# Performance work log

Measured on AMD Instinct MI355X. Metric: run time of the kernel, lower is better.

Reference implementation:

```python
import jax, jax.numpy as jnp
import numpy as np

N, K, D = 32768, 8192, 64  # active voxels, codebook size, embedding dim


def setup_inputs() -> dict:
    key = jax.random.key(0)
    k1, k2 = jax.random.split(key)
    z_feats = jax.random.normal(k1, (N, D), dtype=jnp.float32)
    codebook = jax.random.normal(k2, (K, D), dtype=jnp.float32)  # nn.Embedding weight, N(0,1)
    return {"z_feats": z_feats, "codebook": codebook}


def reference(z_feats, codebook):
    # torch.cdist(z, E) followed by argmin(dim=1). sqrt is monotonic, so argmin over
    # squared Euclidean distances gives identical indices (same math, cheaper).
    # d2[n,k] = ||z_n||^2 - 2 z_n . e_k + ||e_k||^2  -> [N, K] (dominant intermediate)
    d2 = (jnp.sum(z_feats * z_feats, axis=1, keepdims=True)
          - 2.0 * (z_feats @ codebook.T)
          + jnp.sum(codebook * codebook, axis=1))
    encoding_indices = jnp.argmin(d2, axis=1)  # [N]

    quantized_feats = codebook[encoding_indices]  # embedding gather [N, D]

    # F.mse_loss == mean over all elements
    commitment_loss = jnp.mean((z_feats - jax.lax.stop_gradient(quantized_feats)) ** 2)
    vq_loss = jnp.mean((quantized_feats - jax.lax.stop_gradient(z_feats)) ** 2)

    # straight-through estimator
    quantized = z_feats + jax.lax.stop_gradient(quantized_feats - z_feats)
    return quantized, vq_loss, commitment_loss, encoding_indices
```

## Files before the change

### kernel.cpp

```cpp
#include <hip/hip_runtime.h>
#include <cfloat>


typedef __bf16 bf16x8 __attribute__((ext_vector_type(8)));
typedef float  f32x16 __attribute__((ext_vector_type(16)));

constexpr int N_ROWS = 32768;
constexpr int K_CB   = 8192;
constexpr int D_DIM  = 64;
constexpr size_t NQ  = (size_t)N_ROWS * D_DIM;
constexpr int WS_LOSS = K_CB;
constexpr size_t WS_SPLIT_F   = 8448;
constexpr size_t SPLIT_BYTES  = (size_t)K_CB * D_DIM * 4;
constexpr size_t WS_NEED      = WS_SPLIT_F * 4 + SPLIT_BYTES;
constexpr int NROUND = K_CB / 256;

#define GLL16(gp, lp)                                                          \
  __builtin_amdgcn_global_load_lds(                                            \
      (const __attribute__((address_space(1))) unsigned int*)(gp),             \
      (__attribute__((address_space(3))) unsigned int*)(lp), 16, 0, 0)

__global__ __launch_bounds__(256) void vq_prep(const float* __restrict__ cb,
                                               float* __restrict__ ws) {
  const int k = blockIdx.x * 256 + threadIdx.x;
  if (k == 0) ws[WS_LOSS] = 0.0f;
  const float4* p = reinterpret_cast<const float4*>(cb) + (size_t)k * 16;
  float s0 = 0.f, s1 = 0.f, s2 = 0.f, s3 = 0.f;
#pragma unroll
  for (int j = 0; j < 16; ++j) {
    float4 v = p[j];
    s0 = fmaf(v.x, v.x, s0); s1 = fmaf(v.y, v.y, s1);
    s2 = fmaf(v.z, v.z, s2); s3 = fmaf(v.w, v.w, s3);
  }
  ws[k] = (s0 + s1) + (s2 + s3);
}

__global__ __launch_bounds__(256) void vq_split(const float* __restrict__ cb,
                                                float* __restrict__ ws) {
  const int u  = blockIdx.x * 256 + threadIdx.x;
  const int k  = u >> 3, ch = u & 7;
  const int r  = k >> 8, t = (k >> 5) & 7, c = k & 31;
  const float* src = cb + (size_t)k * D_DIM + ch * 8;
  float4 f0 = *reinterpret_cast<const float4*>(src);
  float4 f1 = *reinterpret_cast<const float4*>(src + 4);
  float xs[8] = {f0.x, f0.y, f0.z, f0.w, f1.x, f1.y, f1.z, f1.w};
  bf16x8 hi, lo;
#pragma unroll
  for (int j = 0; j < 8; ++j) {
    __bf16 h = (__bf16)xs[j];
    hi[j] = h;
    lo[j] = (__bf16)(xs[j] - (float)h);
  }
  char* base = reinterpret_cast<char*>(ws + WS_SPLIT_F) +
               (size_t)r * 65536 + (size_t)t * 8192 + (size_t)ch * 512 + (size_t)c * 16;
  *reinterpret_cast<bf16x8*>(base)        = hi;
  *reinterpret_cast<bf16x8*>(base + 4096) = lo;
}

__global__ __launch_bounds__(512, 2) void vq_mfma(const float* __restrict__ z,
                                                  const float* __restrict__ cb,
                                                  float* __restrict__ ws,
                                                  float* __restrict__ out) {
  __shared__ __attribute__((aligned(16))) unsigned char lds[131072];

  const int tid = threadIdx.x;
  const int w = tid >> 6, l = tid & 63;
  const int c = l & 31, g = l >> 5;
  const int rowbase = blockIdx.x * 128;

  bf16x8 zh[4][4], zl[4][4];
#pragma unroll
  for (int q = 0; q < 4; ++q) {
    const float* zr = z + (size_t)(rowbase + q * 32 + c) * D_DIM + 8 * g;
#pragma unroll
    for (int s = 0; s < 4; ++s) {
      float4 f0 = *reinterpret_cast<const float4*>(zr + 16 * s);
      float4 f1 = *reinterpret_cast<const float4*>(zr + 16 * s + 4);
      float xs[8] = {f0.x, f0.y, f0.z, f0.w, f1.x, f1.y, f1.z, f1.w};
#pragma unroll
      for (int j = 0; j < 8; ++j) {
        __bf16 h = (__bf16)xs[j];
        zh[q][s][j] = h;
        zl[q][s][j] = (__bf16)(xs[j] - (float)h);
      }
    }
  }

  const char* sg = reinterpret_cast<const char*>(ws + WS_SPLIT_F) +
                   (size_t)w * 1024 + (size_t)l * 16;

#pragma unroll
  for (int j = 0; j < 8; ++j) GLL16(sg + j * 8192, lds + j * 8192 + w * 1024);
  __syncthreads();

  float best[4];
  int   bpack[4];
#pragma unroll
  for (int q = 0; q < 4; ++q) { best[q] = FLT_MAX; bpack[q] = 0; }

  for (int r = 0; r < NROUND; ++r) {
    const int buf = r & 1;
    if (r < NROUND - 1) {
      const char* s2 = sg + (size_t)(r + 1) * 65536;
      unsigned db = (unsigned)(buf ^ 1) * 65536u;
#pragma unroll
      for (int j = 0; j < 8; ++j)
        GLL16(s2 + j * 8192, lds + db + j * 8192 + w * 1024);
    }

    const unsigned rb = (unsigned)buf * 65536u + (unsigned)w * 8192u +
                        (unsigned)g * 512u + (unsigned)c * 16u;
    f32x16 a0, a1, a2, a3;
#pragma unroll
    for (int i = 0; i < 16; ++i) { a0[i] = 0.f; a1[i] = 0.f; a2[i] = 0.f; a3[i] = 0.f; }

#pragma unroll
    for (int s = 0; s < 4; ++s) {
      bf16x8 ca = *reinterpret_cast<const bf16x8*>(lds + rb + s * 1024);
      bf16x8 cb_ = *reinterpret_cast<const bf16x8*>(lds + rb + s * 1024 + 4096);
      a0 = __builtin_amdgcn_mfma_f32_32x32x16_bf16(ca, zh[0][s], a0, 0, 0, 0);
      a1 = __builtin_amdgcn_mfma_f32_32x32x16_bf16(ca, zh[1][s], a1, 0, 0, 0);
      a2 = __builtin_amdgcn_mfma_f32_32x32x16_bf16(ca, zh[2][s], a2, 0, 0, 0);
      a3 = __builtin_amdgcn_mfma_f32_32x32x16_bf16(ca, zh[3][s], a3, 0, 0, 0);
      a0 = __builtin_amdgcn_mfma_f32_32x32x16_bf16(ca, zl[0][s], a0, 0, 0, 0);
      a1 = __builtin_amdgcn_mfma_f32_32x32x16_bf16(ca, zl[1][s], a1, 0, 0, 0);
      a2 = __builtin_amdgcn_mfma_f32_32x32x16_bf16(ca, zl[2][s], a2, 0, 0, 0);
      a3 = __builtin_amdgcn_mfma_f32_32x32x16_bf16(ca, zl[3][s], a3, 0, 0, 0);
      a0 = __builtin_amdgcn_mfma_f32_32x32x16_bf16(cb_, zh[0][s], a0, 0, 0, 0);
      a1 = __builtin_amdgcn_mfma_f32_32x32x16_bf16(cb_, zh[1][s], a1, 0, 0, 0);
      a2 = __builtin_amdgcn_mfma_f32_32x32x16_bf16(cb_, zh[2][s], a2, 0, 0, 0);
      a3 = __builtin_amdgcn_mfma_f32_32x32x16_bf16(cb_, zh[3][s], a3, 0, 0, 0);
    }

    const float* rp = ws + r * 256 + w * 32 + 4 * g;
    float4 rv0 = *reinterpret_cast<const float4*>(rp);
    float4 rv1 = *reinterpret_cast<const float4*>(rp + 8);
    float4 rv2 = *reinterpret_cast<const float4*>(rp + 16);
    float4 rv3 = *reinterpret_cast<const float4*>(rp + 24);
    float r2v[16] = {rv0.x, rv0.y, rv0.z, rv0.w, rv1.x, rv1.y, rv1.z, rv1.w,
                     rv2.x, rv2.y, rv2.z, rv2.w, rv3.x, rv3.y, rv3.z, rv3.w};
    const int pb = r << 4;
#pragma unroll
    for (int i = 0; i < 16; ++i) {
      float s0 = fmaf(-2.f, a0[i], r2v[i]);
      float s1 = fmaf(-2.f, a1[i], r2v[i]);
      float s2 = fmaf(-2.f, a2[i], r2v[i]);
      float s3 = fmaf(-2.f, a3[i], r2v[i]);
      if (s0 < best[0]) { best[0] = s0; bpack[0] = pb + i; }
      if (s1 < best[1]) { best[1] = s1; bpack[1] = pb + i; }
      if (s2 < best[2]) { best[2] = s2; bpack[2] = pb + i; }
      if (s3 < best[3]) { best[3] = s3; bpack[3] = pb + i; }
    }
    __syncthreads();
  }

  int bk[4];
#pragma unroll
  for (int q = 0; q < 4; ++q) {
    int rr = bpack[q] >> 4, i = bpack[q] & 15;
    int cid = (i & 3) + 8 * (i >> 2) + 4 * g;
    bk[q] = rr * 256 + w * 32 + cid;
  }
#pragma unroll
  for (int q = 0; q < 4; ++q) {
    float ob = __shfl_xor(best[q], 32, 64);
    int   ok = __shfl_xor(bk[q], 32, 64);
    if (ob < best[q] || (ob == best[q] && ok < bk[q])) { best[q] = ob; bk[q] = ok; }
  }

  float* fbuf = reinterpret_cast<float*>(lds);
  int*   kbuf = reinterpret_cast<int*>(lds + 4096);
  int*   ibuf = reinterpret_cast<int*>(lds + 8192);
  if (l < 32) {
#pragma unroll
    for (int q = 0; q < 4; ++q) {
      fbuf[w * 128 + q * 32 + l] = best[q];
      kbuf[w * 128 + q * 32 + l] = bk[q];
    }
  }
  __syncthreads();

  if (tid < 128) {
    float bb = fbuf[tid];
    int   kk = kbuf[tid];
#pragma unroll
    for (int ww = 1; ww < 8; ++ww) {
      float b2 = fbuf[ww * 128 + tid];
      int   k2 = kbuf[ww * 128 + tid];
      if (b2 < bb || (b2 == bb && k2 < kk)) { bb = b2; kk = k2; }
    }
    ibuf[tid] = kk;
    out[NQ + 2 + rowbase + tid] = (float)kk;
  }
  __syncthreads();

  {
    const int row_l = tid >> 2, seg = tid & 3;
    const int idx  = ibuf[row_l];
    const int grow = rowbase + row_l;
    const float4* qp = reinterpret_cast<const float4*>(cb + (size_t)idx * D_DIM + seg * 16);
    const float4* zp = reinterpret_cast<const float4*>(z + (size_t)grow * D_DIM + seg * 16);
    float4*       op = reinterpret_cast<float4*>(out + (size_t)grow * D_DIM + seg * 16);
    float lp = 0.f;
#pragma unroll
    for (int cc = 0; cc < 4; ++cc) {
      float4 qv = qp[cc], zv = zp[cc];
      op[cc] = qv;
      float dx = zv.x - qv.x, dy = zv.y - qv.y;
      float dz = zv.z - qv.z, dw = zv.w - qv.w;
      lp += (dx * dx + dy * dy) + (dz * dz + dw * dw);
    }
#pragma unroll
    for (int off = 32; off > 0; off >>= 1) lp += __shfl_down(lp, off, 64);
    if (l == 0) atomicAdd(ws + WS_LOSS, lp);
  }
}

__global__ __launch_bounds__(512, 2) void vq_main_reg(const float* __restrict__ z,
                                                      const float* __restrict__ cb,
                                                      float* __restrict__ ws,
                                                      float* __restrict__ out) {
  __shared__ __attribute__((aligned(16))) unsigned char lds[65536];
  const int tid = threadIdx.x;
  const int w = tid >> 6, l = tid & 63;
  const int rg = w >> 1, sp = w & 1;
  const int c = l & 31, g = l >> 5;
  const int rowbase = blockIdx.x * 128;
  const int myrow = rowbase + rg * 32 + c;

  bf16x8 zh[4], zl[4];
#pragma unroll
  for (int s = 0; s < 4; ++s) {
    const float* zp = z + (size_t)myrow * D_DIM + 16 * s + 8 * g;
    float4 f0 = *reinterpret_cast<const float4*>(zp);
    float4 f1 = *reinterpret_cast<const float4*>(zp + 4);
    float xs[8] = {f0.x, f0.y, f0.z, f0.w, f1.x, f1.y, f1.z, f1.w};
#pragma unroll
    for (int j = 0; j < 8; ++j) {
      __bf16 h = (__bf16)xs[j];
      zh[s][j] = h;
      zl[s][j] = (__bf16)(xs[j] - (float)h);
    }
  }
  const int st_t01 = tid >> 8;
  const int st_c   = (tid >> 3) & 31;
  const int st_ch  = tid & 7;
  const unsigned st_off = (unsigned)(st_t01 * 16384 + st_ch * 512 + st_c * 16);
  const float* st_g = cb + (size_t)(st_t01 * 32 + st_c) * D_DIM + st_ch * 8;

  float best = FLT_MAX;
  int   bidx = 0;
  float4 p0 = *reinterpret_cast<const float4*>(st_g);
  float4 p1 = *reinterpret_cast<const float4*>(st_g + 4);
  {
    float xs[8] = {p0.x, p0.y, p0.z, p0.w, p1.x, p1.y, p1.z, p1.w};
    bf16x8 hi, lo;
#pragma unroll
    for (int j = 0; j < 8; ++j) {
      __bf16 h = (__bf16)xs[j];
      hi[j] = h; lo[j] = (__bf16)(xs[j] - (float)h);
    }
    *reinterpret_cast<bf16x8*>(lds + st_off)        = hi;
    *reinterpret_cast<bf16x8*>(lds + st_off + 8192) = lo;
  }
  __syncthreads();
  const unsigned rd_base = (unsigned)(sp * 16384 + c * 16);
  for (int r = 0; r < 128; ++r) {
    const int buf = r & 1;
    if (r < 127) {
      const float* gp = st_g + (size_t)(r + 1) * (64 * D_DIM);
      p0 = *reinterpret_cast<const float4*>(gp);
      p1 = *reinterpret_cast<const float4*>(gp + 4);
    }
    const unsigned b0 = (unsigned)buf * 32768u + rd_base;
    bf16x8 ch[4], cl[4];
#pragma unroll
    for (int s = 0; s < 4; ++s) {
      unsigned off = b0 + (unsigned)((2 * s + g) * 512);
      ch[s] = *reinterpret_cast<const bf16x8*>(lds + off);
      cl[s] = *reinterpret_cast<const bf16x8*>(lds + off + 8192);
    }
    f32x16 acc;
#pragma unroll
    for (int i = 0; i < 16; ++i) acc[i] = 0.f;
#pragma unroll
    for (int s = 0; s < 4; ++s) {
      acc = __builtin_amdgcn_mfma_f32_32x32x16_bf16(ch[s], zh[s], acc, 0, 0, 0);
      acc = __builtin_amdgcn_mfma_f32_32x32x16_bf16(ch[s], zl[s], acc, 0, 0, 0);
      acc = __builtin_amdgcn_mfma_f32_32x32x16_bf16(cl[s], zh[s], acc, 0, 0, 0);
    }
    const int tb = (2 * r + sp) * 32 + 4 * g;
#pragma unroll
    for (int q = 0; q < 4; ++q) {
      float4 rv = *reinterpret_cast<const float4*>(ws + tb + 8 * q);
      float ra[4] = {rv.x, rv.y, rv.z, rv.w};
#pragma unroll
      for (int j = 0; j < 4; ++j) {
        float sc = fmaf(-2.f, acc[4 * q + j], ra[j]);
        int kg = tb + 8 * q + j;
        if (sc < best) { best = sc; bidx = kg; }
      }
    }
    if (r < 127) {
      float xs[8] = {p0.x, p0.y, p0.z, p0.w, p1.x, p1.y, p1.z, p1.w};
      bf16x8 hi, lo;
#pragma unroll
      for (int j = 0; j < 8; ++j) {
        __bf16 h = (__bf16)xs[j];
        hi[j] = h; lo[j] = (__bf16)(xs[j] - (float)h);
      }
      unsigned wo = (unsigned)(buf ^ 1) * 32768u + st_off;
      *reinterpret_cast<bf16x8*>(lds + wo)        = hi;
      *reinterpret_cast<bf16x8*>(lds + wo + 8192) = lo;
    }
    __syncthreads();
  }
  {
    float ob = __shfl_xor(best, 32, 64);
    int   oi = __shfl_xor(bidx, 32, 64);
    if (ob < best || (ob == best && oi < bidx)) { best = ob; bidx = oi; }
  }
  float* mf  = reinterpret_cast<float*>(lds);
  int*   mi  = reinterpret_cast<int*>(lds + 1024);
  int*   mix = reinterpret_cast<int*>(lds + 2048);
  if (l < 32) { mf[w * 32 + c] = best; mi[w * 32 + c] = bidx; }
  __syncthreads();
  if (tid < 128) {
    int rgg = tid >> 5, rl = tid & 31;
    float b0 = mf[(2 * rgg) * 32 + rl];     int i0 = mi[(2 * rgg) * 32 + rl];
    float b1 = mf[(2 * rgg + 1) * 32 + rl]; int i1 = mi[(2 * rgg + 1) * 32 + rl];
    int idx = (b1 < b0 || (b1 == b0 && i1 < i0)) ? i1 : i0;
    mix[tid] = idx;
    out[NQ + 2 + rowbase + tid] = (float)idx;
  }
  __syncthreads();
  {
    const int row_l = tid >> 2, seg = tid & 3;
    const int idx  = mix[row_l];
    const int grow = rowbase + row_l;
    const float4* qp = reinterpret_cast<const float4*>(cb + (size_t)idx * D_DIM + seg * 16);
    const float4* zp = reinterpret_cast<const float4*>(z + (size_t)grow * D_DIM + seg * 16);
    float4*       op = reinterpret_cast<float4*>(out + (size_t)grow * D_DIM + seg * 16);
    float lp = 0.f;
#pragma unroll
    for (int cc = 0; cc < 4; ++cc) {
      float4 qv = qp[cc], zv = zp[cc];
      op[cc] = qv;
      float dx = zv.x - qv.x, dy = zv.y - qv.y;
      float dz = zv.z - qv.z, dw = zv.w - qv.w;
      lp += (dx * dx + dy * dy) + (dz * dz + dw * dw);
    }
#pragma unroll
    for (int off = 32; off > 0; off >>= 1) lp += __shfl_down(lp, off, 64);
    if (l == 0) atomicAdd(ws + WS_LOSS, lp);
  }
}

__global__ void vq_fin(const float* __restrict__ ws, float* __restrict__ out) {
  float mm = ws[WS_LOSS] * (1.0f / (float)(N_ROWS * D_DIM));
  out[NQ]     = mm;
  out[NQ + 1] = mm;
}

extern "C" void kernel_launch(void* const* d_in, const int* in_sizes, int n_in,
                              void* d_out, int out_size, void* d_ws, size_t ws_size,
                              hipStream_t stream) {
  (void)in_sizes; (void)n_in; (void)out_size;
  const float* z  = (const float*)d_in[0];
  const float* cb = (const float*)d_in[1];
  float* out = (float*)d_out;
  float* ws  = (float*)d_ws;

  vq_prep<<<K_CB / 256, 256, 0, stream>>>(cb, ws);
  if (ws_size >= WS_NEED) {
    vq_split<<<256, 256, 0, stream>>>(cb, ws);
    vq_mfma<<<N_ROWS / 128, 512, 0, stream>>>(z, cb, ws, out);
  } else {
    vq_main_reg<<<N_ROWS / 128, 512, 0, stream>>>(z, cb, ws, out);
  }
  vq_fin<<<1, 1, 0, stream>>>(ws, out);
}
```

Measured before the change: 144.7 us.

## Halve rows per block and drop LDS double buffering to raise occupancy

The MFMA kernel now handles 64 rows per block instead of 128, uses a single 64 KB LDS buffer instead of a 128 KB double buffer, and declares 4 blocks per CU in launch bounds instead of 2. Each round loads its codebook tile, synchronizes, then computes. Latency hiding now comes from more resident blocks rather than software prefetch. MFMA sections are wrapped in s_setprio to favour matrix issue. In exchange, each block reuses the loaded codebook tile across half as many rows, so total codebook traffic from L2 doubles, and every round now waits on a load with a barrier instead of overlapping it.

```diff
diff --git a/kernel.cpp b/kernel.cpp
--- a/kernel.cpp
+++ b/kernel.cpp
@@ -57,20 +57,20 @@
   *reinterpret_cast<bf16x8*>(base + 4096) = lo;
 }
 
-__global__ __launch_bounds__(512, 2) void vq_mfma(const float* __restrict__ z,
-                                                  const float* __restrict__ cb,
-                                                  float* __restrict__ ws,
-                                                  float* __restrict__ out) {
-  __shared__ __attribute__((aligned(16))) unsigned char lds[131072];
+__global__ __launch_bounds__(512, 4) void vq_mfma8(const float* __restrict__ z,
+                                                   const float* __restrict__ cb,
+                                                   float* __restrict__ ws,
+                                                   float* __restrict__ out) {
+  __shared__ __attribute__((aligned(16))) unsigned char lds[65536];
 
   const int tid = threadIdx.x;
   const int w = tid >> 6, l = tid & 63;
   const int c = l & 31, g = l >> 5;
-  const int rowbase = blockIdx.x * 128;
-
-  bf16x8 zh[4][4], zl[4][4];
-#pragma unroll
-  for (int q = 0; q < 4; ++q) {
+  const int rowbase = blockIdx.x * 64;
+
+  bf16x8 zh[2][4], zl[2][4];
+#pragma unroll
+  for (int q = 0; q < 2; ++q) {
     const float* zr = z + (size_t)(rowbase + q * 32 + c) * D_DIM + 8 * g;
 #pragma unroll
     for (int s = 0; s < 4; ++s) {
@@ -89,48 +89,34 @@
   const char* sg = reinterpret_cast<const char*>(ws + WS_SPLIT_F) +
                    (size_t)w * 1024 + (size_t)l * 16;
 
-#pragma unroll
-  for (int j = 0; j < 8; ++j) GLL16(sg + j * 8192, lds + j * 8192 + w * 1024);
-  __syncthreads();
-
-  float best[4];
-  int   bpack[4];
-#pragma unroll
-  for (int q = 0; q < 4; ++q) { best[q] = FLT_MAX; bpack[q] = 0; }
+  float best0 = FLT_MAX, best1 = FLT_MAX;
+  int   bp0 = 0, bp1 = 0;
 
   for (int r = 0; r < NROUND; ++r) {
-    const int buf = r & 1;
-    if (r < NROUND - 1) {
-      const char* s2 = sg + (size_t)(r + 1) * 65536;
-      unsigned db = (unsigned)(buf ^ 1) * 65536u;
-#pragma unroll
-      for (int j = 0; j < 8; ++j)
-        GLL16(s2 + j * 8192, lds + db + j * 8192 + w * 1024);
-    }
-
-    const unsigned rb = (unsigned)buf * 65536u + (unsigned)w * 8192u +
-                        (unsigned)g * 512u + (unsigned)c * 16u;
-    f32x16 a0, a1, a2, a3;
-#pragma unroll
-    for (int i = 0; i < 16; ++i) { a0[i] = 0.f; a1[i] = 0.f; a2[i] = 0.f; a3[i] = 0.f; }
-
+    const char* s2 = sg + (size_t)r * 65536;
+#pragma unroll
+    for (int j = 0; j < 8; ++j)
+      GLL16(s2 + j * 8192, lds + j * 8192 + w * 1024);
+    __syncthreads();
+
+    const unsigned rb = (unsigned)w * 8192u + (unsigned)g * 512u + (unsigned)c * 16u;
+    f32x16 a0, a1;
+#pragma unroll
+    for (int i = 0; i < 16; ++i) { a0[i] = 0.f; a1[i] = 0.f; }
+
+    __builtin_amdgcn_s_setprio(1);
 #pragma unroll
     for (int s = 0; s < 4; ++s) {
       bf16x8 ca = *reinterpret_cast<const bf16x8*>(lds + rb + s * 1024);
-      bf16x8 cb_ = *reinterpret_cast<const bf16x8*>(lds + rb + s * 1024 + 4096);
+      bf16x8 cl = *reinterpret_cast<const bf16x8*>(lds + rb + s * 1024 + 4096);
       a0 = __builtin_amdgcn_mfma_f32_32x32x16_bf16(ca, zh[0][s], a0, 0, 0, 0);
       a1 = __builtin_amdgcn_mfma_f32_32x32x16_bf16(ca, zh[1][s], a1, 0, 0, 0);
-      a2 = __builtin_amdgcn_mfma_f32_32x32x16_bf16(ca, zh[2][s], a2, 0, 0, 0);
-      a3 = __builtin_amdgcn_mfma_f32_32x32x16_bf16(ca, zh[3][s], a3, 0, 0, 0);
       a0 = __builtin_amdgcn_mfma_f32_32x32x16_bf16(ca, zl[0][s], a0, 0, 0, 0);
       a1 = __builtin_amdgcn_mfma_f32_32x32x16_bf16(ca, zl[1][s], a1, 0, 0, 0);
-      a2 = __builtin_amdgcn_mfma_f32_32x32x16_bf16(ca, zl[2][s], a2, 0, 0, 0);
-      a3 = __builtin_amdgcn_mfma_f32_32x32x16_bf16(ca, zl[3][s], a3, 0, 0, 0);
-      a0 = __builtin_amdgcn_mfma_f32_32x32x16_bf16(cb_, zh[0][s], a0, 0, 0, 0);
-      a1 = __builtin_amdgcn_mfma_f32_32x32x16_bf16(cb_, zh[1][s], a1, 0, 0, 0);
-      a2 = __builtin_amdgcn_mfma_f32_32x32x16_bf16(cb_, zh[2][s], a2, 0, 0, 0);
-      a3 = __builtin_amdgcn_mfma_f32_32x32x16_bf16(cb_, zh[3][s], a3, 0, 0, 0);
-    }
+      a0 = __builtin_amdgcn_mfma_f32_32x32x16_bf16(cl, zh[0][s], a0, 0, 0, 0);
+      a1 = __builtin_amdgcn_mfma_f32_32x32x16_bf16(cl, zh[1][s], a1, 0, 0, 0);
+    }
+    __builtin_amdgcn_s_setprio(0);
 
     const float* rp = ws + r * 256 + w * 32 + 4 * g;
     float4 rv0 = *reinterpret_cast<const float4*>(rp);
@@ -144,49 +130,44 @@
     for (int i = 0; i < 16; ++i) {
       float s0 = fmaf(-2.f, a0[i], r2v[i]);
       float s1 = fmaf(-2.f, a1[i], r2v[i]);
-      float s2 = fmaf(-2.f, a2[i], r2v[i]);
-      float s3 = fmaf(-2.f, a3[i], r2v[i]);
-      if (s0 < best[0]) { best[0] = s0; bpack[0] = pb + i; }
-      if (s1 < best[1]) { best[1] = s1; bpack[1] = pb + i; }
-      if (s2 < best[2]) { best[2] = s2; bpack[2] = pb + i; }
-      if (s3 < best[3]) { best[3] = s3; bpack[3] = pb + i; }
+      if (s0 < best0) { best0 = s0; bp0 = pb + i; }
+      if (s1 < best1) { best1 = s1; bp1 = pb + i; }
     }
     __syncthreads();
   }
 
-  int bk[4];
-#pragma unroll
-  for (int q = 0; q < 4; ++q) {
-    int rr = bpack[q] >> 4, i = bpack[q] & 15;
-    int cid = (i & 3) + 8 * (i >> 2) + 4 * g;
-    bk[q] = rr * 256 + w * 32 + cid;
-  }
-#pragma unroll
-  for (int q = 0; q < 4; ++q) {
-    float ob = __shfl_xor(best[q], 32, 64);
-    int   ok = __shfl_xor(bk[q], 32, 64);
-    if (ob < best[q] || (ob == best[q] && ok < bk[q])) { best[q] = ob; bk[q] = ok; }
+  int bk0, bk1;
+  {
+    int rr = bp0 >> 4, i = bp0 & 15;
+    bk0 = rr * 256 + w * 32 + (i & 3) + 8 * (i >> 2) + 4 * g;
+    rr = bp1 >> 4; i = bp1 & 15;
+    bk1 = rr * 256 + w * 32 + (i & 3) + 8 * (i >> 2) + 4 * g;
+  }
+  {
+    float ob = __shfl_xor(best0, 32, 64);
+    int   ok = __shfl_xor(bk0, 32, 64);
+    if (ob < best0 || (ob == best0 && ok < bk0)) { best0 = ob; bk0 = ok; }
+    ob = __shfl_xor(best1, 32, 64);
+    ok = __shfl_xor(bk1, 32, 64);
+    if (ob < best1 || (ob == best1 && ok < bk1)) { best1 = ob; bk1 = ok; }
   }
 
   float* fbuf = reinterpret_cast<float*>(lds);
-  int*   kbuf = reinterpret_cast<int*>(lds + 4096);
-  int*   ibuf = reinterpret_cast<int*>(lds + 8192);
+  int*   kbuf = reinterpret_cast<int*>(lds + 2048);
+  int*   ibuf = reinterpret_cast<int*>(lds + 4096);
   if (l < 32) {
-#pragma unroll
-    for (int q = 0; q < 4; ++q) {
-      fbuf[w * 128 + q * 32 + l] = best[q];
-      kbuf[w * 128 + q * 32 + l] = bk[q];
-    }
-  }
-  __syncthreads();
-
-  if (tid < 128) {
+    fbuf[w * 64 + c]      = best0;  kbuf[w * 64 + c]      = bk0;
+    fbuf[w * 64 + 32 + c] = best1;  kbuf[w * 64 + 32 + c] = bk1;
+  }
+  __syncthreads();
+
+  if (tid < 64) {
     float bb = fbuf[tid];
     int   kk = kbuf[tid];
 #pragma unroll
     for (int ww = 1; ww < 8; ++ww) {
-      float b2 = fbuf[ww * 128 + tid];
-      int   k2 = kbuf[ww * 128 + tid];
+      float b2 = fbuf[ww * 64 + tid];
+      int   k2 = kbuf[ww * 64 + tid];
       if (b2 < bb || (b2 == bb && k2 < kk)) { bb = b2; kk = k2; }
     }
     ibuf[tid] = kk;
@@ -195,15 +176,15 @@
   __syncthreads();
 
   {
-    const int row_l = tid >> 2, seg = tid & 3;
+    const int row_l = tid >> 3, seg = tid & 7;
     const int idx  = ibuf[row_l];
     const int grow = rowbase + row_l;
-    const float4* qp = reinterpret_cast<const float4*>(cb + (size_t)idx * D_DIM + seg * 16);
-    const float4* zp = reinterpret_cast<const float4*>(z + (size_t)grow * D_DIM + seg * 16);
-    float4*       op = reinterpret_cast<float4*>(out + (size_t)grow * D_DIM + seg * 16);
+    const float4* qp = reinterpret_cast<const float4*>(cb + (size_t)idx * D_DIM + seg * 8);
+    const float4* zp = reinterpret_cast<const float4*>(z + (size_t)grow * D_DIM + seg * 8);
+    float4*       op = reinterpret_cast<float4*>(out + (size_t)grow * D_DIM + seg * 8);
     float lp = 0.f;
 #pragma unroll
-    for (int cc = 0; cc < 4; ++cc) {
+    for (int cc = 0; cc < 2; ++cc) {
       float4 qv = qp[cc], zv = zp[cc];
       op[cc] = qv;
       float dx = zv.x - qv.x, dy = zv.y - qv.y;
@@ -238,8 +219,7 @@
 #pragma unroll
     for (int j = 0; j < 8; ++j) {
       __bf16 h = (__bf16)xs[j];
-      zh[s][j] = h;
-      zl[s][j] = (__bf16)(xs[j] - (float)h);
+      zh[s][j] = h; zl[s][j] = (__bf16)(xs[j] - (float)h);
     }
   }
   const int st_t01 = tid >> 8;
@@ -374,7 +354,7 @@
   vq_prep<<<K_CB / 256, 256, 0, stream>>>(cb, ws);
   if (ws_size >= WS_NEED) {
     vq_split<<<256, 256, 0, stream>>>(cb, ws);
-    vq_mfma<<<N_ROWS / 128, 512, 0, stream>>>(z, cb, ws, out);
+    vq_mfma8<<<N_ROWS / 64, 512, 0, stream>>>(z, cb, ws, out);
   } else {
     vq_main_reg<<<N_ROWS / 128, 512, 0, stream>>>(z, cb, ws, out);
   }
```

Result: slower. 157.9 us (+9.1%).

## Load pre-split codebook tiles directly into registers instead of LDS double-buffering

Applied to the files above, without the earlier changes.

The MFMA kernel no longer stages codebook hi/lo bf16 tiles through a double-buffered LDS region via global_load_lds with a barrier each round. Each wave now reads its own fragments straight from global memory (L2-resident workspace) into registers, prefetching the next round's fragments after issuing the MFMAs. The per-round __syncthreads is removed and s_setprio raises priority around the MFMA block. This cuts LDS use from 128KB to 12KB and drops barriers, at the cost of relying on L2 latency being hidden by one round of compute and extra VGPRs for the prefetched fragments.

```diff
diff --git a/kernel.cpp b/kernel.cpp
--- a/kernel.cpp
+++ b/kernel.cpp
@@ -14,11 +14,6 @@
 constexpr size_t SPLIT_BYTES  = (size_t)K_CB * D_DIM * 4;
 constexpr size_t WS_NEED      = WS_SPLIT_F * 4 + SPLIT_BYTES;
 constexpr int NROUND = K_CB / 256;
-
-#define GLL16(gp, lp)                                                          \
-  __builtin_amdgcn_global_load_lds(                                            \
-      (const __attribute__((address_space(1))) unsigned int*)(gp),             \
-      (__attribute__((address_space(3))) unsigned int*)(lp), 16, 0, 0)
 
 __global__ __launch_bounds__(256) void vq_prep(const float* __restrict__ cb,
                                                float* __restrict__ ws) {
@@ -57,11 +52,11 @@
   *reinterpret_cast<bf16x8*>(base + 4096) = lo;
 }
 
-__global__ __launch_bounds__(512, 2) void vq_mfma(const float* __restrict__ z,
-                                                  const float* __restrict__ cb,
-                                                  float* __restrict__ ws,
-                                                  float* __restrict__ out) {
-  __shared__ __attribute__((aligned(16))) unsigned char lds[131072];
+__global__ __launch_bounds__(512, 2) void vq_gd(const float* __restrict__ z,
+                                                const float* __restrict__ cb,
+                                                float* __restrict__ ws,
+                                                float* __restrict__ out) {
+  __shared__ __attribute__((aligned(16))) unsigned char lds[12288];
 
   const int tid = threadIdx.x;
   const int w = tid >> 6, l = tid & 63;
@@ -86,12 +81,16 @@
     }
   }
 
-  const char* sg = reinterpret_cast<const char*>(ws + WS_SPLIT_F) +
-                   (size_t)w * 1024 + (size_t)l * 16;
-
-#pragma unroll
-  for (int j = 0; j < 8; ++j) GLL16(sg + j * 8192, lds + j * 8192 + w * 1024);
-  __syncthreads();
+  const char* hp = reinterpret_cast<const char*>(ws + WS_SPLIT_F) +
+                   (size_t)w * 8192 + (size_t)g * 512 + (size_t)c * 16;
+  const char* lq = hp + 4096;
+
+  bf16x8 fh[4], fl[4];
+#pragma unroll
+  for (int s = 0; s < 4; ++s) {
+    fh[s] = *reinterpret_cast<const bf16x8*>(hp + s * 1024);
+    fl[s] = *reinterpret_cast<const bf16x8*>(lq + s * 1024);
+  }
 
   float best[4];
   int   bpack[4];
@@ -99,37 +98,35 @@
   for (int q = 0; q < 4; ++q) { best[q] = FLT_MAX; bpack[q] = 0; }
 
   for (int r = 0; r < NROUND; ++r) {
-    const int buf = r & 1;
+    f32x16 a0, a1, a2, a3;
+#pragma unroll
+    for (int i = 0; i < 16; ++i) { a0[i] = 0.f; a1[i] = 0.f; a2[i] = 0.f; a3[i] = 0.f; }
+
+    __builtin_amdgcn_s_setprio(1);
+#pragma unroll
+    for (int s = 0; s < 4; ++s) {
+      a0 = __builtin_amdgcn_mfma_f32_32x32x16_bf16(fh[s], zh[0][s], a0, 0, 0, 0);
+      a1 = __builtin_amdgcn_mfma_f32_32x32x16_bf16(fh[s], zh[1][s], a1, 0, 0, 0);
+      a2 = __builtin_amdgcn_mfma_f32_32x32x16_bf16(fh[s], zh[2][s], a2, 0, 0, 0);
+      a3 = __builtin_amdgcn_mfma_f32_32x32x16_bf16(fh[s], zh[3][s], a3, 0, 0, 0);
+      a0 = __builtin_amdgcn_mfma_f32_32x32x16_bf16(fh[s], zl[0][s], a0, 0, 0, 0);
+      a1 = __builtin_amdgcn_mfma_f32_32x32x16_bf16(fh[s], zl[1][s], a1, 0, 0, 0);
+      a2 = __builtin_amdgcn_mfma_f32_32x32x16_bf16(fh[s], zl[2][s], a2, 0, 0, 0);
+      a3 = __builtin_amdgcn_mfma_f32_32x32x16_bf16(fh[s], zl[3][s], a3, 0, 0, 0);
+      a0 = __builtin_amdgcn_mfma_f32_32x32x16_bf16(fl[s], zh[0][s], a0, 0, 0, 0);
+      a1 = __builtin_amdgcn_mfma_f32_32x32x16_bf16(fl[s], zh[1][s], a1, 0, 0, 0);
+      a2 = __builtin_amdgcn_mfma_f32_32x32x16_bf16(fl[s], zh[2][s], a2, 0, 0, 0);
+      a3 = __builtin_amdgcn_mfma_f32_32x32x16_bf16(fl[s], zh[3][s], a3, 0, 0, 0);
+    }
+    __builtin_amdgcn_s_setprio(0);
+
     if (r < NROUND - 1) {
-      const char* s2 = sg + (size_t)(r + 1) * 65536;
-      unsigned db = (unsigned)(buf ^ 1) * 65536u;
-#pragma unroll
-      for (int j = 0; j < 8; ++j)
-        GLL16(s2 + j * 8192, lds + db + j * 8192 + w * 1024);
-    }
-
-    const unsigned rb = (unsigned)buf * 65536u + (unsigned)w * 8192u +
-                        (unsigned)g * 512u + (unsigned)c * 16u;
-    f32x16 a0, a1, a2, a3;
-#pragma unroll
-    for (int i = 0; i < 16; ++i) { a0[i] = 0.f; a1[i] = 0.f; a2[i] = 0.f; a3[i] = 0.f; }
-
-#pragma unroll
-    for (int s = 0; s < 4; ++s) {
-      bf16x8 ca = *reinterpret_cast<const bf16x8*>(lds + rb + s * 1024);
-      bf16x8 cb_ = *reinterpret_cast<const bf16x8*>(lds + rb + s * 1024 + 4096);
-      a0 = __builtin_amdgcn_mfma_f32_32x32x16_bf16(ca, zh[0][s], a0, 0, 0, 0);
-      a1 = __builtin_amdgcn_mfma_f32_32x32x16_bf16(ca, zh[1][s], a1, 0, 0, 0);
-      a2 = __builtin_amdgcn_mfma_f32_32x32x16_bf16(ca, zh[2][s], a2, 0, 0, 0);
-      a3 = __builtin_amdgcn_mfma_f32_32x32x16_bf16(ca, zh[3][s], a3, 0, 0, 0);
-      a0 = __builtin_amdgcn_mfma_f32_32x32x16_bf16(ca, zl[0][s], a0, 0, 0, 0);
-      a1 = __builtin_amdgcn_mfma_f32_32x32x16_bf16(ca, zl[1][s], a1, 0, 0, 0);
-      a2 = __builtin_amdgcn_mfma_f32_32x32x16_bf16(ca, zl[2][s], a2, 0, 0, 0);
-      a3 = __builtin_amdgcn_mfma_f32_32x32x16_bf16(ca, zl[3][s], a3, 0, 0, 0);
-      a0 = __builtin_amdgcn_mfma_f32_32x32x16_bf16(cb_, zh[0][s], a0, 0, 0, 0);
-      a1 = __builtin_amdgcn_mfma_f32_32x32x16_bf16(cb_, zh[1][s], a1, 0, 0, 0);
-      a2 = __builtin_amdgcn_mfma_f32_32x32x16_bf16(cb_, zh[2][s], a2, 0, 0, 0);
-      a3 = __builtin_amdgcn_mfma_f32_32x32x16_bf16(cb_, zh[3][s], a3, 0, 0, 0);
+      hp += 65536; lq += 65536;
+#pragma unroll
+      for (int s = 0; s < 4; ++s) {
+        fh[s] = *reinterpret_cast<const bf16x8*>(hp + s * 1024);
+        fl[s] = *reinterpret_cast<const bf16x8*>(lq + s * 1024);
+      }
     }
 
     const float* rp = ws + r * 256 + w * 32 + 4 * g;
@@ -151,7 +148,6 @@
       if (s2 < best[2]) { best[2] = s2; bpack[2] = pb + i; }
       if (s3 < best[3]) { best[3] = s3; bpack[3] = pb + i; }
     }
-    __syncthreads();
   }
 
   int bk[4];
@@ -238,8 +234,7 @@
 #pragma unroll
     for (int j = 0; j < 8; ++j) {
       __bf16 h = (__bf16)xs[j];
-      zh[s][j] = h;
-      zl[s][j] = (__bf16)(xs[j] - (float)h);
+      zh[s][j] = h; zl[s][j] = (__bf16)(xs[j] - (float)h);
     }
   }
   const int st_t01 = tid >> 8;
@@ -374,7 +369,7 @@
   vq_prep<<<K_CB / 256, 256, 0, stream>>>(cb, ws);
   if (ws_size >= WS_NEED) {
     vq_split<<<256, 256, 0, stream>>>(cb, ws);
-    vq_mfma<<<N_ROWS / 128, 512, 0, stream>>>(z, cb, ws, out);
+    vq_gd<<<N_ROWS / 128, 512, 0, stream>>>(z, cb, ws, out);
   } else {
     vq_main_reg<<<N_ROWS / 128, 512, 0, stream>>>(z, cb, ws, out);
   }
```

Result: faster. 139.8 us (-3.4%).
